# Kernel tuning notes

Hardware: AMD Instinct MI355X
Metric: run time of the kernel (lower is better)

Reference implementation:

```python
import jax, jax.numpy as jnp
import numpy as np

C = 512
GROUPS = 32
EPS = 1e-6

def setup_inputs() -> dict:
    key = jax.random.key(0)
    ks = jax.random.split(key, 8)
    b, h, w = 8, 64, 64
    s = 0.02
    return {
        "x": jax.random.normal(ks[0], (b, C, h, w), dtype=jnp.float32),
        "gn_gamma": jnp.ones((C,), jnp.float32),
        "gn_beta": jnp.zeros((C,), jnp.float32),
        "q_w": jax.random.normal(ks[1], (C, C), jnp.float32) * s,
        "q_b": jnp.zeros((C,), jnp.float32),
        "k_w": jax.random.normal(ks[2], (C, C), jnp.float32) * s,
        "k_b": jnp.zeros((C,), jnp.float32),
        "proj_w": jax.random.normal(ks[3], (C, C), jnp.float32) * s,
        "proj_b": jnp.zeros((C,), jnp.float32),
    }

def _group_norm(x, gamma, beta):
    b, c, h, w = x.shape
    xg = x.reshape(b, GROUPS, c // GROUPS, h, w)
    mu = jnp.mean(xg, axis=(2, 3, 4), keepdims=True)
    var = jnp.var(xg, axis=(2, 3, 4), keepdims=True)
    xn = ((xg - mu) * jax.lax.rsqrt(var + EPS)).reshape(b, c, h, w)
    return xn * gamma[None, :, None, None] + beta[None, :, None, None]

def _conv1x1(x, w, b):
    # x: (b,c,h,w), w: (out,in) -> (b,out,h,w)
    return jnp.einsum('bchw,oc->bohw', x, w) + b[None, :, None, None]

def reference(x, gn_gamma, gn_beta, q_w, q_b, k_w, k_b, proj_w, proj_b):
    b, c, h, w = x.shape
    r = _group_norm(x, gn_gamma, gn_beta)
    q = _conv1x1(r, q_w, q_b).reshape(b, c, h * w)   # (b,c,n)
    k = _conv1x1(r, k_w, k_b).reshape(b, c, h * w)   # (b,c,m)
    v = k  # faithful to source: v = self.k0(r)
    scale = jnp.asarray(c, x.dtype) ** -0.5
    scores = jnp.einsum('bcn,bcm->bnm', q, k) * scale  # (b,n,m)
    attn = jax.nn.softmax(scores, axis=-1)
    out = jnp.einsum('bcm,bnm->bcn', v, attn).reshape(b, c, h, w)
    out = _conv1x1(out, proj_w, proj_b)
    return x + out
```

## Files before the change

### kernel.cpp

```cpp
#include <hip/hip_runtime.h>
#include <hip/hip_bf16.h>
#include <cstdint>

#define DEVI __device__ __forceinline__

typedef __attribute__((ext_vector_type(8))) short short8;
typedef __attribute__((ext_vector_type(4))) float f32x4;
typedef unsigned int u32;
typedef unsigned short u16;

DEVI u16 f2bf(float f) {
  __hip_bfloat16 h = __float2bfloat16(f);
  return *reinterpret_cast<u16*>(&h);
}

DEVI void async_cp16(const __hip_bfloat16* g, __hip_bfloat16* l) {
  __builtin_amdgcn_global_load_lds(
      (const __attribute__((address_space(1))) u32*)(uintptr_t)g,
      (__attribute__((address_space(3))) u32*)(uintptr_t)l, 16, 0, 0);
}

DEVI void xcd_remap(int& bx, int& by, int& bz) {
  const int gx = gridDim.x, gy = gridDim.y;
  const int d = blockIdx.x + gx * (blockIdx.y + gridDim.y * blockIdx.z);
  const int idx = d >> 3;
  const int g = (d & 7) + 8 * (idx / gx);
  bx = idx % gx;
  by = g % gy;
  bz = g / gy;
}


template<int BIAS_MODE, bool EXPSUM>
__global__ __launch_bounds__(512, 2) void gemm256_tn(
    const __hip_bfloat16* __restrict__ A, int lda, size_t sA,
    const __hip_bfloat16* __restrict__ B, int ldb, size_t sB,
    void* __restrict__ Zv, int ldz, size_t sZ,
    const float* __restrict__ bias,
    float alpha, int K,
    float* __restrict__ rsum)
{
  __shared__ __hip_bfloat16 ls[3 * 16384];
  const int t  = threadIdx.x;
  const int bb = blockIdx.z;

  const int nbxy = gridDim.x * gridDim.y;
  const int borig = blockIdx.y * gridDim.x + blockIdx.x;
  const int cpx = nbxy >> 3;
  const int blog = (borig & 7) * cpx + (borig >> 3);
  const int bx = blog % gridDim.x;
  const int by = blog / gridDim.x;
  const int n0 = bx * 256;
  const int m0 = by * 256;

  const __hip_bfloat16* Ab = A + (size_t)bb * sA;
  const __hip_bfloat16* Bb = B + (size_t)bb * sB;

  const int lane = t & 63;
  const int quad = lane >> 4;
  const int l16  = lane & 15;
  const int wave = t >> 6;
  const int wm   = (wave >> 2) * 128;
  const int wn   = (wave & 3) * 64;
  const int qa   = (quad ^ (l16 & 3)) * 8;

  const int rowc = t >> 2;
  const int kc   = ((t & 3) ^ (rowc & 3)) * 8;
  const __hip_bfloat16* ga0 = Ab + (size_t)(m0 + rowc) * lda + kc;
  const __hip_bfloat16* ga1 = Ab + (size_t)(m0 + rowc + 128) * lda + kc;
  const __hip_bfloat16* gb0 = Bb + (size_t)(n0 + rowc) * ldb + kc;
  const __hip_bfloat16* gb1 = Bb + (size_t)(n0 + rowc + 128) * ldb + kc;

  f32x4 acc[8][4] = {};

#define STAGE256(SLOT)                                                        \
  {                                                                           \
    __hip_bfloat16* lb = ls + (SLOT) * 16384 + t * 8;                         \
    async_cp16(ga0, lb);                                                      \
    async_cp16(ga1, lb + 4096);                                               \
    async_cp16(gb0, lb + 8192);                                               \
    async_cp16(gb1, lb + 12288);                                              \
    ga0 += 32; ga1 += 32; gb0 += 32; gb1 += 32;                               \
  }

#define COMPUTE256(SLOT)                                                      \
  {                                                                           \
    const __hip_bfloat16* bA = ls + (SLOT) * 16384;                           \
    const __hip_bfloat16* bB = bA + 8192;                                     \
    short8 af[8], bfr[4];                                                     \
    _Pragma("unroll")                                                         \
    for (int i = 0; i < 8; ++i)                                               \
      af[i] = *(const short8*)(bA + (wm + i * 16 + l16) * 32 + qa);           \
    _Pragma("unroll")                                                         \
    for (int j = 0; j < 4; ++j)                                               \
      bfr[j] = *(const short8*)(bB + (wn + j * 16 + l16) * 32 + qa);          \
    _Pragma("unroll")                                                         \
    for (int i = 0; i < 8; ++i)                                               \
      _Pragma("unroll")                                                       \
      for (int j = 0; j < 4; ++j)                                             \
        acc[i][j] = __builtin_amdgcn_mfma_f32_16x16x32_bf16(af[i], bfr[j],    \
                                                            acc[i][j], 0, 0, 0); \
  }

  STAGE256(0);
  STAGE256(1);
  const int nk = K >> 5;
  for (int kw = 0; kw < nk - 1; ++kw) {
    asm volatile("s_waitcnt vmcnt(4)" ::: "memory");
    __builtin_amdgcn_s_barrier();
    if (kw + 2 < nk) {
      const int ss = (kw + 2) % 3;
      STAGE256(ss);
    }
    const int sc = kw % 3;
    COMPUTE256(sc);
  }
  asm volatile("s_waitcnt vmcnt(0)" ::: "memory");
  __builtin_amdgcn_s_barrier();
  COMPUTE256((nk - 1) % 3);

#undef STAGE256
#undef COMPUTE256

  if (EXPSUM) {
    __syncthreads();
    float* rs = (float*)ls;
    if (t < 256) rs[t] = 0.f;
    __syncthreads();
    float lsum[4] = {0.f, 0.f, 0.f, 0.f};
#pragma unroll
    for (int i = 0; i < 8; ++i) {
#pragma unroll
      for (int j = 0; j < 4; ++j) {
        const int m = m0 + wm + i * 16 + quad * 4;
        const int n = n0 + wn + j * 16 + l16;
        f32x4 v = acc[i][j];
        v[0] = __expf(v[0] * alpha); v[1] = __expf(v[1] * alpha);
        v[2] = __expf(v[2] * alpha); v[3] = __expf(v[3] * alpha);
        lsum[j] += v[0] + v[1] + v[2] + v[3];
        union { u16 s[4]; uint2 q; } pk;
        pk.s[0] = f2bf(v[0]); pk.s[1] = f2bf(v[1]);
        pk.s[2] = f2bf(v[2]); pk.s[3] = f2bf(v[3]);
        *(uint2*)((__hip_bfloat16*)Zv + (size_t)bb * sZ + (size_t)n * ldz + m) = pk.q;
      }
    }
#pragma unroll
    for (int j = 0; j < 4; ++j)
      atomicAdd(&rs[wn + j * 16 + l16], lsum[j]);
    __syncthreads();
    if (t < 256) atomicAdd(rsum + (size_t)bb * 4096 + n0 + t, rs[t]);
    return;
  }

#pragma unroll
  for (int i = 0; i < 8; ++i) {
#pragma unroll
    for (int j = 0; j < 4; ++j) {
      const int m = m0 + wm + i * 16 + quad * 4;
      const int n = n0 + wn + j * 16 + l16;
      f32x4 v = acc[i][j];
      if (BIAS_MODE == 1) v += *(const f32x4*)(bias + m);
      else if (BIAS_MODE == 2) v += bias[n];
      v *= alpha;
      union { u16 s[4]; uint2 q; } pk;
      pk.s[0] = f2bf(v[0]); pk.s[1] = f2bf(v[1]);
      pk.s[2] = f2bf(v[2]); pk.s[3] = f2bf(v[3]);
      *(uint2*)((__hip_bfloat16*)Zv + (size_t)bb * sZ + (size_t)n * ldz + m) = pk.q;
    }
  }
}

__global__ __launch_bounds__(256, 2) void gemm128_final(
    const __hip_bfloat16* __restrict__ A, int lda, size_t sA,
    const __hip_bfloat16* __restrict__ B, int ldb, size_t sB,
    float* __restrict__ out, int ldz, size_t sZ,
    const float* __restrict__ bias,
    int K,
    const float* __restrict__ rsum,
    const float* __restrict__ xres)
{
  __shared__ __hip_bfloat16 ls[5 * 8192];
  const int t = threadIdx.x;

  int bx, by, bb;
  xcd_remap(bx, by, bb);
  const int n0 = bx * 128;
  const int m0 = by * 128;

  const __hip_bfloat16* Ab = A + (size_t)bb * sA;
  const __hip_bfloat16* Bb = B + (size_t)bb * sB;

  const int lane = t & 63;
  const int quad = lane >> 4;
  const int l16  = lane & 15;
  const int wave = t >> 6;
  const int wm   = (wave >> 1) * 64;
  const int wn   = (wave & 1) * 64;
  const int qa   = (quad ^ (l16 & 3)) * 8;

  const int rowc = t >> 2;
  const int kc   = ((t & 3) ^ (rowc & 3)) * 8;
  const __hip_bfloat16* ga0 = Ab + (size_t)(m0 + rowc) * lda + kc;
  const __hip_bfloat16* ga1 = Ab + (size_t)(m0 + rowc + 64) * lda + kc;
  const __hip_bfloat16* gb0 = Bb + (size_t)(n0 + rowc) * ldb + kc;
  const __hip_bfloat16* gb1 = Bb + (size_t)(n0 + rowc + 64) * ldb + kc;

  f32x4 acc[4][4] = {};

#define STAGE128(SLOT)                                                        \
  {                                                                           \
    __hip_bfloat16* lb = ls + (SLOT) * 8192 + t * 8;                          \
    async_cp16(ga0, lb);                                                      \
    async_cp16(ga1, lb + 2048);                                               \
    async_cp16(gb0, lb + 4096);                                               \
    async_cp16(gb1, lb + 6144);                                               \
    ga0 += 32; ga1 += 32; gb0 += 32; gb1 += 32;                               \
  }

#define COMPUTE128(SLOT)                                                      \
  {                                                                           \
    const __hip_bfloat16* bA = ls + (SLOT) * 8192;                            \
    const __hip_bfloat16* bB = bA + 4096;                                     \
    short8 af[4], bfr[4];                                                     \
    _Pragma("unroll")                                                         \
    for (int i = 0; i < 4; ++i)                                               \
      af[i] = *(const short8*)(bA + (wm + i * 16 + l16) * 32 + qa);           \
    _Pragma("unroll")                                                         \
    for (int j = 0; j < 4; ++j)                                               \
      bfr[j] = *(const short8*)(bB + (wn + j * 16 + l16) * 32 + qa);          \
    _Pragma("unroll")                                                         \
    for (int i = 0; i < 4; ++i)                                               \
      _Pragma("unroll")                                                       \
      for (int j = 0; j < 4; ++j)                                             \
        acc[i][j] = __builtin_amdgcn_mfma_f32_16x16x32_bf16(af[i], bfr[j],    \
                                                            acc[i][j], 0, 0, 0); \
  }

  STAGE128(0);
  STAGE128(1);
  STAGE128(2);
  STAGE128(3);
  const int nk = K >> 5;
  for (int kw = 0; kw < nk - 4; ++kw) {
    asm volatile("s_waitcnt vmcnt(12)" ::: "memory");
    __builtin_amdgcn_s_barrier();
    STAGE128((kw + 4) % 5);
    COMPUTE128(kw % 5);
  }
  asm volatile("s_waitcnt vmcnt(12)" ::: "memory");
  __builtin_amdgcn_s_barrier();
  COMPUTE128((nk - 4) % 5);
  asm volatile("s_waitcnt vmcnt(8)" ::: "memory");
  __builtin_amdgcn_s_barrier();
  COMPUTE128((nk - 3) % 5);
  asm volatile("s_waitcnt vmcnt(4)" ::: "memory");
  __builtin_amdgcn_s_barrier();
  COMPUTE128((nk - 2) % 5);
  asm volatile("s_waitcnt vmcnt(0)" ::: "memory");
  __builtin_amdgcn_s_barrier();
  COMPUTE128((nk - 1) % 5);

#undef STAGE128
#undef COMPUTE128

#pragma unroll
  for (int i = 0; i < 4; ++i) {
#pragma unroll
    for (int j = 0; j < 4; ++j) {
      const int m = m0 + wm + i * 16 + quad * 4;
      const int n = n0 + wn + j * 16 + l16;
      f32x4 v = acc[i][j];
      const size_t zoff = (size_t)n * ldz + m;
      f32x4 rs = *(const f32x4*)(rsum + (size_t)bb * 4096 + m);
      f32x4 xx = *(const f32x4*)(xres + (size_t)bb * sZ + zoff);
      const float pbv = bias[n];
      v[0] = xx[0] + pbv + v[0] / rs[0];
      v[1] = xx[1] + pbv + v[1] / rs[1];
      v[2] = xx[2] + pbv + v[2] / rs[2];
      v[3] = xx[3] + pbv + v[3] / rs[3];
      *(f32x4*)(out + (size_t)bb * sZ + zoff) = v;
    }
  }
}

__global__ __launch_bounds__(256) void gn_stats(const float* __restrict__ x,
                                                float2* __restrict__ stats) {
  const int bg = blockIdx.x;
  const f32x4* p = (const f32x4*)(x + (size_t)bg * 65536);
  float s = 0.f, s2 = 0.f;
  for (int i = threadIdx.x; i < 16384; i += 256) {
    f32x4 v = p[i];
    s  += v[0] + v[1] + v[2] + v[3];
    s2 += v[0]*v[0] + v[1]*v[1] + v[2]*v[2] + v[3]*v[3];
  }
  for (int o = 32; o > 0; o >>= 1) { s += __shfl_down(s, o); s2 += __shfl_down(s2, o); }
  __shared__ float ws[4], ws2[4];
  const int wave = threadIdx.x >> 6;
  if ((threadIdx.x & 63) == 0) { ws[wave] = s; ws2[wave] = s2; }
  __syncthreads();
  if (threadIdx.x == 0) {
    float S  = ws[0] + ws[1] + ws[2] + ws[3];
    float S2 = ws2[0] + ws2[1] + ws2[2] + ws2[3];
    float mu = S * (1.f / 65536.f);
    float var = S2 * (1.f / 65536.f) - mu * mu;
    stats[bg] = make_float2(mu, rsqrtf(var + 1e-6f));
  }
}

__global__ __launch_bounds__(256) void gn_apply(const float* __restrict__ x,
                                                const float2* __restrict__ stats,
                                                const float* __restrict__ gamma,
                                                const float* __restrict__ beta,
                                                __hip_bfloat16* __restrict__ rt) {
  const int b = blockIdx.y, n0 = blockIdx.x * 64;
  __shared__ float tile[64][65];
  const int t  = threadIdx.x;
  const int cl = t >> 2;
  const int q4 = (t & 3) * 4;
  for (int cc = 0; cc < 8; ++cc) {
    const int c = cc * 64 + cl;
    const float2 ms = stats[b * 32 + (c >> 4)];
    const float ga = gamma[c] * ms.y;
    const float be = beta[c] - ms.x * ga;
    const float* src = x + ((size_t)b * 512 + c) * 4096 + n0;
#pragma unroll
    for (int p = 0; p < 4; ++p) {
      f32x4 v = *(const f32x4*)(src + q4 + p * 16);
      tile[cl][q4 + p * 16 + 0] = fmaf(v[0], ga, be);
      tile[cl][q4 + p * 16 + 1] = fmaf(v[1], ga, be);
      tile[cl][q4 + p * 16 + 2] = fmaf(v[2], ga, be);
      tile[cl][q4 + p * 16 + 3] = fmaf(v[3], ga, be);
    }
    __syncthreads();
    const int nw = t >> 2;
    const int cw = (t & 3) * 16;
    union { u16 s[16]; uint4 q[2]; } pk;
#pragma unroll
    for (int j = 0; j < 16; ++j) pk.s[j] = f2bf(tile[cw + j][nw]);
    __hip_bfloat16* dst = rt + ((size_t)b * 4096 + n0 + nw) * 512 + cc * 64 + cw;
    *(uint4*)dst = pk.q[0];
    *((uint4*)dst + 1) = pk.q[1];
    __syncthreads();
  }
}

__global__ __launch_bounds__(256) void prep(
    const float* __restrict__ qw, const float* __restrict__ kw,
    const float* __restrict__ pw, const float* __restrict__ qb,
    const float* __restrict__ kb,
    __hip_bfloat16* __restrict__ wqk, __hip_bfloat16* __restrict__ wp,
    float* __restrict__ bias_qk, float* __restrict__ rsum) {
  const int blk = blockIdx.x;
  if (blk < 768) {
    const float* src = (blk < 256) ? qw : (blk < 512) ? kw : pw;
    __hip_bfloat16* dst = (blk < 256) ? wqk : (blk < 512) ? (wqk + 262144) : wp;
    const int i = ((blk & 255) * 256 + threadIdx.x) * 4;
    f32x4 v = *(const f32x4*)(src + i);
    union { u16 s4[4]; uint2 q; } pk;
    pk.s4[0] = f2bf(v[0]); pk.s4[1] = f2bf(v[1]);
    pk.s4[2] = f2bf(v[2]); pk.s4[3] = f2bf(v[3]);
    *(uint2*)(dst + i) = pk.q;
  } else if (blk == 768) {
    const int i = threadIdx.x * 4;
    *(f32x4*)(bias_qk + i) = *(const f32x4*)(qb + i);
    *(f32x4*)(bias_qk + 512 + i) = *(const f32x4*)(kb + i);
  } else {
    ((f32x4*)rsum)[(blk - 769) * 256 + threadIdx.x] = f32x4{0.f, 0.f, 0.f, 0.f};
  }
}

extern "C" void kernel_launch(void* const* d_in, const int* in_sizes, int n_in,
                              void* d_out, int out_size, void* d_ws, size_t ws_size,
                              hipStream_t stream) {
  const float* x     = (const float*)d_in[0];
  const float* gamma = (const float*)d_in[1];
  const float* beta  = (const float*)d_in[2];
  const float* q_w   = (const float*)d_in[3];
  const float* q_b   = (const float*)d_in[4];
  const float* k_w   = (const float*)d_in[5];
  const float* k_b   = (const float*)d_in[6];
  const float* p_w   = (const float*)d_in[7];
  const float* p_b   = (const float*)d_in[8];
  float* out = (float*)d_out;

  constexpr int B = 8, C = 512, N = 4096;
  constexpr size_t NC = (size_t)N * C;
  constexpr size_t NN = (size_t)N * N;

  char* ws = (char*)d_ws;
  size_t off = 0;
  auto alloc = [&](size_t bytes) {
    void* p = ws + off;
    off += (bytes + 255) & ~(size_t)255;
    return p;
  };

  __hip_bfloat16* wqk = (__hip_bfloat16*)alloc((size_t)1024 * 512 * 2);
  __hip_bfloat16* wp  = (__hip_bfloat16*)alloc((size_t)C * C * 2);
  float* bias_qk      = (float*)alloc(1024 * 4);
  float2* stats       = (float2*)alloc((size_t)B * 32 * sizeof(float2));
  float* rsum         = (float*)alloc((size_t)B * N * 4);
  __hip_bfloat16* rt  = (__hip_bfloat16*)alloc(B * NC * 2);
  __hip_bfloat16* qkt = (__hip_bfloat16*)alloc(B * (size_t)N * 1024 * 2);
  __hip_bfloat16* wpv = (__hip_bfloat16*)alloc(B * NC * 2);
  const size_t base_off = off;

  const size_t attn_b_bytes = NN * 2;
  size_t avail = (ws_size > base_off) ? ws_size - base_off : 0;
  int G = 4;
  if (avail < 4 * attn_b_bytes) G = 2;
  if (avail < 2 * attn_b_bytes) G = 1;
  __hip_bfloat16* attn = (__hip_bfloat16*)alloc(attn_b_bytes * G);

  const dim3 blk(256);
  const dim3 blk512(512);
  const float scale = 0.044194173824159216f;

  prep<<<dim3(801), blk, 0, stream>>>(q_w, k_w, p_w, q_b, k_b,
                                      wqk, wp, bias_qk, rsum);

  gn_stats<<<dim3(B * 32), blk, 0, stream>>>(x, stats);
  gn_apply<<<dim3(64, B), blk, 0, stream>>>(x, stats, gamma, beta, rt);

  gemm256_tn<1, false><<<dim3(16, 4, B), blk512, 0, stream>>>(
      wqk, C, 0, rt, C, NC, qkt, 1024, (size_t)N * 1024,
      bias_qk, 1.f, C, nullptr);

  gemm256_tn<0, false><<<dim3(2, 16, B), blk512, 0, stream>>>(
      qkt + 512, 1024, (size_t)N * 1024, wp, C, 0,
      wpv, N, NC, nullptr, 1.f, C, nullptr);

  for (int b0 = 0; b0 < B; ) {
    const int Gc = (B - b0 < G) ? (B - b0) : G;

    gemm256_tn<0, true><<<dim3(16, 16, Gc), blk512, 0, stream>>>(
        qkt + (size_t)b0 * N * 1024 + 512, 1024, (size_t)N * 1024,
        qkt + (size_t)b0 * N * 1024,       1024, (size_t)N * 1024,
        attn, N, NN, nullptr, scale, C, rsum + (size_t)b0 * N);

    gemm128_final<<<dim3(4, 32, Gc), blk, 0, stream>>>(
        attn, N, NN, wpv + (size_t)b0 * NC, N, NC,
        out + (size_t)b0 * NC, N, NC, p_b, N,
        rsum + (size_t)b0 * N, x + (size_t)b0 * NC);

    b0 += Gc;
  }
}
```

Before: 706.0 us.

## Enlarge final PV GEMM tile to 256x128 and fuse GN stats into prep

The final attention-times-value GEMM now uses 256x128 output tiles instead of 128x128. Each wave holds 8x4 accumulators and the five-stage async LDS pipeline moves six 16-byte copies per stage, with the vmcnt thresholds adjusted to match. This roughly halves re-reads of the wpv operand and halves the block count, at the cost of more LDS, more registers and occupancy limited to one block per SIMD group. Separately, the group-norm statistics kernel is merged into the weight-prep kernel to save one launch.

```diff
diff --git a/kernel.cpp b/kernel.cpp
--- a/kernel.cpp
+++ b/kernel.cpp
@@ -170,7 +170,7 @@
   }
 }
 
-__global__ __launch_bounds__(256, 2) void gemm128_final(
+__global__ __launch_bounds__(256, 1) void gemm256x128_final(
     const __hip_bfloat16* __restrict__ A, int lda, size_t sA,
     const __hip_bfloat16* __restrict__ B, int ldb, size_t sB,
     float* __restrict__ out, int ldz, size_t sZ,
@@ -179,13 +179,13 @@
     const float* __restrict__ rsum,
     const float* __restrict__ xres)
 {
-  __shared__ __hip_bfloat16 ls[5 * 8192];
+  __shared__ __hip_bfloat16 ls[5 * 12288];
   const int t = threadIdx.x;
 
   int bx, by, bb;
   xcd_remap(bx, by, bb);
   const int n0 = bx * 128;
-  const int m0 = by * 128;
+  const int m0 = by * 256;
 
   const __hip_bfloat16* Ab = A + (size_t)bb * sA;
   const __hip_bfloat16* Bb = B + (size_t)bb * sB;
@@ -194,7 +194,7 @@
   const int quad = lane >> 4;
   const int l16  = lane & 15;
   const int wave = t >> 6;
-  const int wm   = (wave >> 1) * 64;
+  const int wm   = (wave >> 1) * 128;
   const int wn   = (wave & 1) * 64;
   const int qa   = (quad ^ (l16 & 3)) * 8;
 
@@ -202,69 +202,73 @@
   const int kc   = ((t & 3) ^ (rowc & 3)) * 8;
   const __hip_bfloat16* ga0 = Ab + (size_t)(m0 + rowc) * lda + kc;
   const __hip_bfloat16* ga1 = Ab + (size_t)(m0 + rowc + 64) * lda + kc;
+  const __hip_bfloat16* ga2 = Ab + (size_t)(m0 + rowc + 128) * lda + kc;
+  const __hip_bfloat16* ga3 = Ab + (size_t)(m0 + rowc + 192) * lda + kc;
   const __hip_bfloat16* gb0 = Bb + (size_t)(n0 + rowc) * ldb + kc;
   const __hip_bfloat16* gb1 = Bb + (size_t)(n0 + rowc + 64) * ldb + kc;
 
-  f32x4 acc[4][4] = {};
-
-#define STAGE128(SLOT)                                                        \
+  f32x4 acc[8][4] = {};
+
+#define STAGEPV(SLOT)                                                         \
   {                                                                           \
-    __hip_bfloat16* lb = ls + (SLOT) * 8192 + t * 8;                          \
+    __hip_bfloat16* lb = ls + (SLOT) * 12288 + t * 8;                         \
     async_cp16(ga0, lb);                                                      \
     async_cp16(ga1, lb + 2048);                                               \
-    async_cp16(gb0, lb + 4096);                                               \
-    async_cp16(gb1, lb + 6144);                                               \
-    ga0 += 32; ga1 += 32; gb0 += 32; gb1 += 32;                               \
-  }
-
-#define COMPUTE128(SLOT)                                                      \
+    async_cp16(ga2, lb + 4096);                                               \
+    async_cp16(ga3, lb + 6144);                                               \
+    async_cp16(gb0, lb + 8192);                                               \
+    async_cp16(gb1, lb + 10240);                                              \
+    ga0 += 32; ga1 += 32; ga2 += 32; ga3 += 32; gb0 += 32; gb1 += 32;         \
+  }
+
+#define COMPUTEPV(SLOT)                                                       \
   {                                                                           \
-    const __hip_bfloat16* bA = ls + (SLOT) * 8192;                            \
-    const __hip_bfloat16* bB = bA + 4096;                                     \
-    short8 af[4], bfr[4];                                                     \
-    _Pragma("unroll")                                                         \
-    for (int i = 0; i < 4; ++i)                                               \
+    const __hip_bfloat16* bA = ls + (SLOT) * 12288;                           \
+    const __hip_bfloat16* bB = bA + 8192;                                     \
+    short8 af[8], bfr[4];                                                     \
+    _Pragma("unroll")                                                         \
+    for (int i = 0; i < 8; ++i)                                               \
       af[i] = *(const short8*)(bA + (wm + i * 16 + l16) * 32 + qa);           \
     _Pragma("unroll")                                                         \
     for (int j = 0; j < 4; ++j)                                               \
       bfr[j] = *(const short8*)(bB + (wn + j * 16 + l16) * 32 + qa);          \
     _Pragma("unroll")                                                         \
-    for (int i = 0; i < 4; ++i)                                               \
+    for (int i = 0; i < 8; ++i)                                               \
       _Pragma("unroll")                                                       \
       for (int j = 0; j < 4; ++j)                                             \
         acc[i][j] = __builtin_amdgcn_mfma_f32_16x16x32_bf16(af[i], bfr[j],    \
                                                             acc[i][j], 0, 0, 0); \
   }
 
-  STAGE128(0);
-  STAGE128(1);
-  STAGE128(2);
-  STAGE128(3);
+  STAGEPV(0);
+  STAGEPV(1);
+  STAGEPV(2);
+  STAGEPV(3);
   const int nk = K >> 5;
   for (int kw = 0; kw < nk - 4; ++kw) {
-    asm volatile("s_waitcnt vmcnt(12)" ::: "memory");
+    asm volatile("s_waitcnt vmcnt(18)" ::: "memory");
     __builtin_amdgcn_s_barrier();
-    STAGE128((kw + 4) % 5);
-    COMPUTE128(kw % 5);
-  }
+    STAGEPV((kw + 4) % 5);
+    COMPUTEPV(kw % 5);
+  }
+  asm volatile("s_waitcnt vmcnt(18)" ::: "memory");
+  __builtin_amdgcn_s_barrier();
+  COMPUTEPV((nk - 4) % 5);
   asm volatile("s_waitcnt vmcnt(12)" ::: "memory");
   __builtin_amdgcn_s_barrier();
-  COMPUTE128((nk - 4) % 5);
-  asm volatile("s_waitcnt vmcnt(8)" ::: "memory");
+  COMPUTEPV((nk - 3) % 5);
+  asm volatile("s_waitcnt vmcnt(6)" ::: "memory");
   __builtin_amdgcn_s_barrier();
-  COMPUTE128((nk - 3) % 5);
-  asm volatile("s_waitcnt vmcnt(4)" ::: "memory");
-  __builtin_amdgcn_s_barrier();
-  COMPUTE128((nk - 2) % 5);
+  COMPUTEPV((nk - 2) % 5);
   asm volatile("s_waitcnt vmcnt(0)" ::: "memory");
   __builtin_amdgcn_s_barrier();
-  COMPUTE128((nk - 1) % 5);
-
-#undef STAGE128
-#undef COMPUTE128
-
-#pragma unroll
-  for (int i = 0; i < 4; ++i) {
+  COMPUTEPV((nk - 1) % 5);
+
+#undef STAGEPV
+#undef COMPUTEPV
+
+#pragma unroll
+  for (int i = 0; i < 8; ++i) {
 #pragma unroll
     for (int j = 0; j < 4; ++j) {
       const int m = m0 + wm + i * 16 + quad * 4;
@@ -283,27 +287,50 @@
   }
 }
 
-__global__ __launch_bounds__(256) void gn_stats(const float* __restrict__ x,
-                                                float2* __restrict__ stats) {
-  const int bg = blockIdx.x;
-  const f32x4* p = (const f32x4*)(x + (size_t)bg * 65536);
-  float s = 0.f, s2 = 0.f;
-  for (int i = threadIdx.x; i < 16384; i += 256) {
-    f32x4 v = p[i];
-    s  += v[0] + v[1] + v[2] + v[3];
-    s2 += v[0]*v[0] + v[1]*v[1] + v[2]*v[2] + v[3]*v[3];
-  }
-  for (int o = 32; o > 0; o >>= 1) { s += __shfl_down(s, o); s2 += __shfl_down(s2, o); }
-  __shared__ float ws[4], ws2[4];
-  const int wave = threadIdx.x >> 6;
-  if ((threadIdx.x & 63) == 0) { ws[wave] = s; ws2[wave] = s2; }
-  __syncthreads();
-  if (threadIdx.x == 0) {
-    float S  = ws[0] + ws[1] + ws[2] + ws[3];
-    float S2 = ws2[0] + ws2[1] + ws2[2] + ws2[3];
-    float mu = S * (1.f / 65536.f);
-    float var = S2 * (1.f / 65536.f) - mu * mu;
-    stats[bg] = make_float2(mu, rsqrtf(var + 1e-6f));
+__global__ __launch_bounds__(256) void prep_stats(
+    const float* __restrict__ qw, const float* __restrict__ kw,
+    const float* __restrict__ pw, const float* __restrict__ qb,
+    const float* __restrict__ kb,
+    __hip_bfloat16* __restrict__ wqk, __hip_bfloat16* __restrict__ wp,
+    float* __restrict__ bias_qk, float* __restrict__ rsum,
+    const float* __restrict__ x, float2* __restrict__ stats) {
+  const int blk = blockIdx.x;
+  if (blk < 768) {
+    const float* src = (blk < 256) ? qw : (blk < 512) ? kw : pw;
+    __hip_bfloat16* dst = (blk < 256) ? wqk : (blk < 512) ? (wqk + 262144) : wp;
+    const int i = ((blk & 255) * 256 + threadIdx.x) * 4;
+    f32x4 v = *(const f32x4*)(src + i);
+    union { u16 s4[4]; uint2 q; } pk;
+    pk.s4[0] = f2bf(v[0]); pk.s4[1] = f2bf(v[1]);
+    pk.s4[2] = f2bf(v[2]); pk.s4[3] = f2bf(v[3]);
+    *(uint2*)(dst + i) = pk.q;
+  } else if (blk == 768) {
+    const int i = threadIdx.x * 4;
+    *(f32x4*)(bias_qk + i) = *(const f32x4*)(qb + i);
+    *(f32x4*)(bias_qk + 512 + i) = *(const f32x4*)(kb + i);
+  } else if (blk < 801) {
+    ((f32x4*)rsum)[(blk - 769) * 256 + threadIdx.x] = f32x4{0.f, 0.f, 0.f, 0.f};
+  } else {
+    const int bg = blk - 801;
+    const f32x4* p = (const f32x4*)(x + (size_t)bg * 65536);
+    float s = 0.f, s2 = 0.f;
+    for (int i = threadIdx.x; i < 16384; i += 256) {
+      f32x4 v = p[i];
+      s  += v[0] + v[1] + v[2] + v[3];
+      s2 += v[0]*v[0] + v[1]*v[1] + v[2]*v[2] + v[3]*v[3];
+    }
+    for (int o = 32; o > 0; o >>= 1) { s += __shfl_down(s, o); s2 += __shfl_down(s2, o); }
+    __shared__ float wsum[4], wsum2[4];
+    const int wave = threadIdx.x >> 6;
+    if ((threadIdx.x & 63) == 0) { wsum[wave] = s; wsum2[wave] = s2; }
+    __syncthreads();
+    if (threadIdx.x == 0) {
+      float S  = wsum[0] + wsum[1] + wsum[2] + wsum[3];
+      float S2 = wsum2[0] + wsum2[1] + wsum2[2] + wsum2[3];
+      float mu = S * (1.f / 65536.f);
+      float var = S2 * (1.f / 65536.f) - mu * mu;
+      stats[bg] = make_float2(mu, rsqrtf(var + 1e-6f));
+    }
   }
 }
 
@@ -344,31 +371,6 @@
   }
 }
 
-__global__ __launch_bounds__(256) void prep(
-    const float* __restrict__ qw, const float* __restrict__ kw,
-    const float* __restrict__ pw, const float* __restrict__ qb,
-    const float* __restrict__ kb,
-    __hip_bfloat16* __restrict__ wqk, __hip_bfloat16* __restrict__ wp,
-    float* __restrict__ bias_qk, float* __restrict__ rsum) {
-  const int blk = blockIdx.x;
-  if (blk < 768) {
-    const float* src = (blk < 256) ? qw : (blk < 512) ? kw : pw;
-    __hip_bfloat16* dst = (blk < 256) ? wqk : (blk < 512) ? (wqk + 262144) : wp;
-    const int i = ((blk & 255) * 256 + threadIdx.x) * 4;
-    f32x4 v = *(const f32x4*)(src + i);
-    union { u16 s4[4]; uint2 q; } pk;
-    pk.s4[0] = f2bf(v[0]); pk.s4[1] = f2bf(v[1]);
-    pk.s4[2] = f2bf(v[2]); pk.s4[3] = f2bf(v[3]);
-    *(uint2*)(dst + i) = pk.q;
-  } else if (blk == 768) {
-    const int i = threadIdx.x * 4;
-    *(f32x4*)(bias_qk + i) = *(const f32x4*)(qb + i);
-    *(f32x4*)(bias_qk + 512 + i) = *(const f32x4*)(kb + i);
-  } else {
-    ((f32x4*)rsum)[(blk - 769) * 256 + threadIdx.x] = f32x4{0.f, 0.f, 0.f, 0.f};
-  }
-}
-
 extern "C" void kernel_launch(void* const* d_in, const int* in_sizes, int n_in,
                               void* d_out, int out_size, void* d_ws, size_t ws_size,
                               hipStream_t stream) {
@@ -416,10 +418,9 @@
   const dim3 blk512(512);
   const float scale = 0.044194173824159216f;
 
-  prep<<<dim3(801), blk, 0, stream>>>(q_w, k_w, p_w, q_b, k_b,
-                                      wqk, wp, bias_qk, rsum);
-
-  gn_stats<<<dim3(B * 32), blk, 0, stream>>>(x, stats);
+  prep_stats<<<dim3(801 + B * 32), blk, 0, stream>>>(
+      q_w, k_w, p_w, q_b, k_b, wqk, wp, bias_qk, rsum, x, stats);
+
   gn_apply<<<dim3(64, B), blk, 0, stream>>>(x, stats, gamma, beta, rt);
 
   gemm256_tn<1, false><<<dim3(16, 4, B), blk512, 0, stream>>>(
@@ -438,7 +439,7 @@
         qkt + (size_t)b0 * N * 1024,       1024, (size_t)N * 1024,
         attn, N, NN, nullptr, scale, C, rsum + (size_t)b0 * N);
 
-    gemm128_final<<<dim3(4, 32, Gc), blk, 0, stream>>>(
+    gemm256x128_final<<<dim3(4, 16, Gc), blk, 0, stream>>>(
         attn, N, NN, wpv + (size_t)b0 * NC, N, NC,
         out + (size_t)b0 * NC, N, NC, p_b, N,
         rsum + (size_t)b0 * N, x + (size_t)b0 * NC);
```

Result: slower. 897.5 us (+27.1%).
